# Kernel tuning notes

Measured on AMD Instinct MI355X. Metric: run time of the kernel, lower is better.

## Reference

```python
import jax, jax.numpy as jnp
import numpy as np

B, T, D_IN, H, C = 256, 2048, 64, 32, 16
RHO, SPARSITY = 0.9, 0.1


def _reservoir(rng, n):
    # uniform(-1,1), scale to spectral radius RHO, then sparsify (same order as torch code)
    W = rng.uniform(-1.0, 1.0, (n, n)).astype(np.float32)
    W *= RHO / np.max(np.abs(np.linalg.eigvals(W)))
    W *= (rng.random((n, n)) < SPARSITY).astype(np.float32)
    return jnp.asarray(W)


def _linear(rng, fan_in, fan_out):
    bound = 1.0 / np.sqrt(fan_in)
    W = rng.uniform(-bound, bound, (fan_out, fan_in)).astype(np.float32)
    b = rng.uniform(-bound, bound, (fan_out,)).astype(np.float32)
    return jnp.asarray(W), jnp.asarray(b)


def setup_inputs() -> dict:
    key = jax.random.key(0)
    rng = np.random.default_rng(0)
    x = jax.random.normal(key, (B, T, D_IN), dtype=jnp.float32)
    # frozen encoder input / reservoir weights (uniform(-1,1) weights, default-init biases)
    W_in = jnp.asarray(rng.uniform(-1.0, 1.0, (H, D_IN)).astype(np.float32))
    b_in = jnp.asarray(rng.uniform(-1 / np.sqrt(D_IN), 1 / np.sqrt(D_IN), (H,)).astype(np.float32))
    W_res_enc = _reservoir(rng, H)
    b_res_enc = jnp.asarray(rng.uniform(-1 / np.sqrt(H), 1 / np.sqrt(H), (H,)).astype(np.float32))
    W_code, b_code = _linear(rng, H, C)
    W_co, b_co = _linear(rng, C, H)
    W_res_dec = _reservoir(rng, H)
    b_res_dec = jnp.asarray(rng.uniform(-1 / np.sqrt(H), 1 / np.sqrt(H), (H,)).astype(np.float32))
    W_ro, b_ro = _linear(rng, H, D_IN)
    return dict(x=x, W_in=W_in, b_in=b_in, W_res_enc=W_res_enc, b_res_enc=b_res_enc,
                W_code=W_code, b_code=b_code, W_co=W_co, b_co=b_co,
                W_res_dec=W_res_dec, b_res_dec=b_res_dec, W_ro=W_ro, b_ro=b_ro)


def reference(x, W_in, b_in, W_res_enc, b_res_enc, W_code, b_code, W_co, b_co,
              W_res_dec, b_res_dec, W_ro, b_ro):
    Bs = x.shape[0]
    h0 = jnp.zeros((Bs, W_res_enc.shape[0]), dtype=x.dtype)
    # precompute input projection for all timesteps: [T, B, H]
    u_enc = jnp.swapaxes(jnp.einsum('btd,hd->bth', x, W_in) + b_in, 0, 1)

    def enc_step(h, u):
        h = jnp.tanh(u + h @ W_res_enc.T + b_res_enc)
        return h, h

    _, enc = jax.lax.scan(enc_step, h0, u_enc)
    enc = jnp.swapaxes(enc, 0, 1)                      # [B, T, H]

    z = enc @ W_code.T + b_code                        # [B, T, C]
    h_dec_in = z @ W_co.T + b_co                       # [B, T, H]

    def dec_step(h, u):
        h = jnp.tanh(u + h @ W_res_dec.T + b_res_dec)
        return h, h

    _, dec = jax.lax.scan(dec_step, h0, jnp.swapaxes(h_dec_in, 0, 1))
    dec = jnp.swapaxes(dec, 0, 1)                      # [B, T, H]
    return dec @ W_ro.T + b_ro                         # [B, T, D_IN]
```

## Files before the change

kernel.cpp:

```cpp
#include <hip/hip_runtime.h>
#include <math.h>

#define B_    256
#define T_    2048
#define DIN   64
#define H_    32
#define C_    16

#define CHUNK 128
#define WARM  96
#define NCHUNK (T_ / CHUNK)

#define OFF_U 0u

__device__ __forceinline__ float fast_tanh(float x) {
    float e2 = __expf(x + x);
    return 1.0f - 2.0f * __builtin_amdgcn_rcpf(e2 + 1.0f);
}

__global__ __launch_bounds__(256) void inproj_kernel(
        const float* __restrict__ x, const float* __restrict__ W_in,
        const float* __restrict__ b_in, const float* __restrict__ b_res_enc,
        float* __restrict__ u) {
    __shared__ __align__(16) float4 lx[128 * 16];

    int tid  = threadIdx.x;
    int w    = tid >> 6;
    int lane = tid & 63;
    int i    = lane & 31;
    int par  = lane >> 5;

    float Wr[DIN];
    {
        const float4* wi4 = reinterpret_cast<const float4*>(W_in + i * DIN);
#pragma unroll
        for (int q = 0; q < DIN / 4; ++q) {
            float4 v = wi4[q];
            Wr[4*q+0] = v.x; Wr[4*q+1] = v.y; Wr[4*q+2] = v.z; Wr[4*q+3] = v.w;
        }
    }
    float bi = b_in[i] + b_res_enc[i];

    long row_base = (long)blockIdx.x * 128;
    const float4* xg = reinterpret_cast<const float4*>(x) + row_base * 16;

#pragma unroll
    for (int k = 0; k < 8; ++k)
        lx[tid + 256 * k] = xg[tid + 256 * k];
    __syncthreads();

#pragma unroll
    for (int g = 0; g < 4; ++g) {
        int r0 = w * 32 + g * 8 + par;
        float acc0 = 0.f, acc1 = 0.f, acc2 = 0.f, acc3 = 0.f;
#pragma unroll
        for (int k4 = 0; k4 < 16; ++k4) {
            float4 wv = { Wr[4*k4+0], Wr[4*k4+1], Wr[4*k4+2], Wr[4*k4+3] };
            float4 x0 = lx[(r0 + 0) * 16 + k4];
            float4 x1 = lx[(r0 + 2) * 16 + k4];
            float4 x2 = lx[(r0 + 4) * 16 + k4];
            float4 x3 = lx[(r0 + 6) * 16 + k4];
            acc0 += x0.x * wv.x + x0.y * wv.y + x0.z * wv.z + x0.w * wv.w;
            acc1 += x1.x * wv.x + x1.y * wv.y + x1.z * wv.z + x1.w * wv.w;
            acc2 += x2.x * wv.x + x2.y * wv.y + x2.z * wv.z + x2.w * wv.w;
            acc3 += x3.x * wv.x + x3.y * wv.y + x3.z * wv.z + x3.w * wv.w;
        }
        long rg = row_base + r0;
        u[(rg + 0) * H_ + i] = acc0 + bi;
        u[(rg + 2) * H_ + i] = acc1 + bi;
        u[(rg + 4) * H_ + i] = acc2 + bi;
        u[(rg + 6) * H_ + i] = acc3 + bi;
    }
}

__global__ __launch_bounds__(64, 4) void scan_kernel(
        const float* __restrict__ u,
        const float* __restrict__ W_res_enc,
        const float* __restrict__ W_res_dec, const float* __restrict__ b_res_dec,
        const float* __restrict__ W_code, const float* __restrict__ b_code,
        const float* __restrict__ W_co,   const float* __restrict__ b_co,
        float* __restrict__ hd ) {
    int lane = threadIdx.x;
    int i = lane & 31;
    int p = lane >> 5;
    int b = blockIdx.x & (B_ - 1);
    int c = blockIdx.x >> 8;
    int t0 = c * CHUNK;
    int tstart = (c == 0) ? 0 : (t0 - WARM);
    int tend = t0 + CHUNK;

    __shared__ __align__(16) float wcode[C_ * H_];
    {
        const float4* src = reinterpret_cast<const float4*>(W_code);
        float4* dst = reinterpret_cast<float4*>(wcode);
        dst[lane]      = src[lane];
        dst[lane + 64] = src[lane + 64];
    }

    float We[16], Wd[16], Wco_r[C_];
    {
        const float4* we4 = reinterpret_cast<const float4*>(W_res_enc + i * H_ + p * 16);
        const float4* wd4 = reinterpret_cast<const float4*>(W_res_dec + i * H_ + p * 16);
        const float4* wc4 = reinterpret_cast<const float4*>(W_co + i * C_);
#pragma unroll
        for (int q = 0; q < 4; ++q) {
            float4 a = we4[q], d = wd4[q], w = wc4[q];
            We[4*q+0]=a.x; We[4*q+1]=a.y; We[4*q+2]=a.z; We[4*q+3]=a.w;
            Wd[4*q+0]=d.x; Wd[4*q+1]=d.y; Wd[4*q+2]=d.z; Wd[4*q+3]=d.w;
            Wco_r[4*q+0]=w.x; Wco_r[4*q+1]=w.y; Wco_r[4*q+2]=w.z; Wco_r[4*q+3]=w.w;
        }
    }
    __syncthreads();

    float Wc[16];
#pragma unroll
    for (int k = 0; k < 16; ++k) {
        float s = 0.f;
#pragma unroll
        for (int cc = 0; cc < C_; ++cc)
            s += Wco_r[cc] * wcode[cc * H_ + p * 16 + k];
        Wc[k] = s;
    }
    float bcd;
    {
        float s = b_co[i] + b_res_dec[i];
#pragma unroll
        for (int cc = 0; cc < C_; ++cc)
            s += Wco_r[cc] * b_code[cc];
        bcd = s;
    }

    float he[16], hdv[16];
#pragma unroll
    for (int k = 0; k < 16; ++k) { he[k] = 0.f; hdv[k] = 0.f; }

    __shared__ __align__(16) float lhe[H_];
    __shared__ __align__(16) float lhd[H_];

    const float* ub = u  + ((long)b * T_) * H_ + i;
    float*       hb = hd + ((long)b * T_) * DIN + i;

    float ucur = ub[(long)tstart * H_];
    float un1  = ub[(long)(tstart + 1) * H_];
    float un2  = ub[(long)(tstart + 2) * H_];

    for (int t = tstart; t < t0; ++t) {
        float e0 = 0.f, e1 = 0.f, e2 = 0.f, e3 = 0.f;
#pragma unroll
        for (int k = 0; k < 16; k += 4) {
            e0 += We[k+0] * he[k+0];
            e1 += We[k+1] * he[k+1];
            e2 += We[k+2] * he[k+2];
            e3 += We[k+3] * he[k+3];
        }
        float ep = (e0 + e1) + (e2 + e3);
        float a = fast_tanh(ep + __shfl_xor(ep, 32) + ucur);
        lhe[i] = a;
        __syncthreads();
        {
            const float4* s4 = reinterpret_cast<const float4*>(&lhe[p * 16]);
#pragma unroll
            for (int q = 0; q < 4; ++q) {
                float4 v = s4[q];
                he[4*q+0]=v.x; he[4*q+1]=v.y; he[4*q+2]=v.z; he[4*q+3]=v.w;
            }
        }
        float g0 = 0.f, g1 = 0.f, d0 = 0.f, d1 = 0.f;
#pragma unroll
        for (int k = 0; k < 16; k += 2) {
            g0 += Wc[k+0] * he[k+0];
            g1 += Wc[k+1] * he[k+1];
            d0 += Wd[k+0] * hdv[k+0];
            d1 += Wd[k+1] * hdv[k+1];
        }
        float part = (g0 + g1) + (d0 + d1);
        float d = fast_tanh(part + __shfl_xor(part, 32) + bcd);
        ucur = un1; un1 = un2;
        un2 = ub[(long)(t + 3) * H_];
        lhd[i] = d;
        __syncthreads();
        {
            const float4* s4 = reinterpret_cast<const float4*>(&lhd[p * 16]);
#pragma unroll
            for (int q = 0; q < 4; ++q) {
                float4 v = s4[q];
                hdv[4*q+0]=v.x; hdv[4*q+1]=v.y; hdv[4*q+2]=v.z; hdv[4*q+3]=v.w;
            }
        }
    }

    for (int t = t0; t < tend; ++t) {
        float e0 = 0.f, e1 = 0.f, e2 = 0.f, e3 = 0.f;
#pragma unroll
        for (int k = 0; k < 16; k += 4) {
            e0 += We[k+0] * he[k+0];
            e1 += We[k+1] * he[k+1];
            e2 += We[k+2] * he[k+2];
            e3 += We[k+3] * he[k+3];
        }
        float ep = (e0 + e1) + (e2 + e3);
        float a = fast_tanh(ep + __shfl_xor(ep, 32) + ucur);
        lhe[i] = a;
        __syncthreads();
        {
            const float4* s4 = reinterpret_cast<const float4*>(&lhe[p * 16]);
#pragma unroll
            for (int q = 0; q < 4; ++q) {
                float4 v = s4[q];
                he[4*q+0]=v.x; he[4*q+1]=v.y; he[4*q+2]=v.z; he[4*q+3]=v.w;
            }
        }
        float g0 = 0.f, g1 = 0.f, d0 = 0.f, d1 = 0.f;
#pragma unroll
        for (int k = 0; k < 16; k += 2) {
            g0 += Wc[k+0] * he[k+0];
            g1 += Wc[k+1] * he[k+1];
            d0 += Wd[k+0] * hdv[k+0];
            d1 += Wd[k+1] * hdv[k+1];
        }
        float part = (g0 + g1) + (d0 + d1);
        float d = fast_tanh(part + __shfl_xor(part, 32) + bcd);
        int tn = t + 3; if (tn > tend - 1) tn = tend - 1;
        ucur = un1; un1 = un2;
        un2 = ub[(long)tn * H_];
        if (p == 0) hb[(long)t * DIN] = d;
        lhd[i] = d;
        __syncthreads();
        {
            const float4* s4 = reinterpret_cast<const float4*>(&lhd[p * 16]);
#pragma unroll
            for (int q = 0; q < 4; ++q) {
                float4 v = s4[q];
                hdv[4*q+0]=v.x; hdv[4*q+1]=v.y; hdv[4*q+2]=v.z; hdv[4*q+3]=v.w;
            }
        }
    }
}

__global__ __launch_bounds__(256) void outproj_kernel(
        const float* __restrict__ W_ro, const float* __restrict__ b_ro,
        float* __restrict__ out) {
    __shared__ __align__(16) float4 lh[128 * 8];

    int tid  = threadIdx.x;
    int w    = tid >> 6;
    int o    = tid & 63;

    float Wo[H_];
    {
        const float4* wo4 = reinterpret_cast<const float4*>(W_ro + o * H_);
#pragma unroll
        for (int q = 0; q < H_ / 4; ++q) {
            float4 v = wo4[q];
            Wo[4*q+0] = v.x; Wo[4*q+1] = v.y; Wo[4*q+2] = v.z; Wo[4*q+3] = v.w;
        }
    }
    float bo = b_ro[o];

    long row_base = (long)blockIdx.x * 128;
    const float4* hg = reinterpret_cast<const float4*>(out);

#pragma unroll
    for (int k = 0; k < 4; ++k) {
        int idx = tid + 256 * k;
        int r = idx >> 3, q = idx & 7;
        lh[idx] = hg[(row_base + r) * 16 + q];
    }
    __syncthreads();

    float* ob = out + (row_base + (long)w * 32) * DIN + o;
#pragma unroll 4
    for (int r = 0; r < 32; ++r) {
        int rr = w * 32 + r;
        float s0 = bo, s1 = 0.f, s2 = 0.f, s3 = 0.f;
#pragma unroll
        for (int q = 0; q < 8; ++q) {
            float4 h4 = lh[rr * 8 + q];
            s0 += Wo[4*q+0] * h4.x;
            s1 += Wo[4*q+1] * h4.y;
            s2 += Wo[4*q+2] * h4.z;
            s3 += Wo[4*q+3] * h4.w;
        }
        __builtin_nontemporal_store((s0 + s1) + (s2 + s3), ob + (long)r * DIN);
    }
}

extern "C" void kernel_launch(void* const* d_in, const int* in_sizes, int n_in,
                              void* d_out, int out_size, void* d_ws, size_t ws_size,
                              hipStream_t stream) {
    const float* x         = (const float*)d_in[0];
    const float* W_in      = (const float*)d_in[1];
    const float* b_in      = (const float*)d_in[2];
    const float* W_res_enc = (const float*)d_in[3];
    const float* b_res_enc = (const float*)d_in[4];
    const float* W_code    = (const float*)d_in[5];
    const float* b_code    = (const float*)d_in[6];
    const float* W_co      = (const float*)d_in[7];
    const float* b_co      = (const float*)d_in[8];
    const float* W_res_dec = (const float*)d_in[9];
    const float* b_res_dec = (const float*)d_in[10];
    const float* W_ro      = (const float*)d_in[11];
    const float* b_ro      = (const float*)d_in[12];
    float* out = (float*)d_out;

    float* u = (float*)((char*)d_ws + OFF_U);

    inproj_kernel<<<(B_ * T_) / 128, 256, 0, stream>>>(x, W_in, b_in, b_res_enc, u);
    scan_kernel<<<B_ * NCHUNK, 64, 0, stream>>>(u, W_res_enc,
                                                W_res_dec, b_res_dec,
                                                W_code, b_code, W_co, b_co, out);
    outproj_kernel<<<(B_ * T_) / 128, 256, 0, stream>>>(W_ro, b_ro, out);
}
```

Measured before the change: 494.2 us.

## Skew decoder one step behind encoder to merge barriers per timestep

The recurrent scan now computes the decoder state for step t-1 in the same iteration as the encoder state for step t. Both tanh results are written together as a float2 into one shared buffer, so each timestep needs one barrier instead of two. This shortens the serial dependency chain and exposes more instruction-level parallelism. The input prefetch no longer clamps its index, so it reads a few rows past the end of each chunk, which for the final chunk lands beyond the buffer.

```diff
diff --git a/kernel.cpp b/kernel.cpp
--- a/kernel.cpp
+++ b/kernel.cpp
@@ -70,6 +70,49 @@
         u[(rg + 2) * H_ + i] = acc1 + bi;
         u[(rg + 4) * H_ + i] = acc2 + bi;
         u[(rg + 6) * H_ + i] = acc3 + bi;
+    }
+}
+
+template<bool DEC, bool STORE>
+__device__ __forceinline__ void esn_step(
+        const float (&We)[16], const float (&Wc)[16], const float (&Wd)[16],
+        float (&he)[16], float (&hdv)[16],
+        float ucur, float bcd, int i, int p,
+        float2* lad, float* sp) {
+    float e0 = 0.f, e1 = 0.f, e2 = 0.f, e3 = 0.f;
+#pragma unroll
+    for (int k = 0; k < 16; k += 4) {
+        e0 += We[k+0] * he[k+0];
+        e1 += We[k+1] * he[k+1];
+        e2 += We[k+2] * he[k+2];
+        e3 += We[k+3] * he[k+3];
+    }
+    float ep = (e0 + e1) + (e2 + e3);
+    float gp = 0.f;
+    if (DEC) {
+        float g0 = 0.f, g1 = 0.f, g2 = 0.f, g3 = 0.f;
+#pragma unroll
+        for (int k = 0; k < 16; k += 2) {
+            g0 += Wc[k+0] * he[k+0];
+            g1 += Wc[k+1] * he[k+1];
+            g2 += Wd[k+0] * hdv[k+0];
+            g3 += Wd[k+1] * hdv[k+1];
+        }
+        gp = (g0 + g1) + (g2 + g3);
+    }
+    float ef = ep + __shfl_xor(ep, 32) + ucur;
+    float gf = gp + __shfl_xor(gp, 32) + bcd;
+    float a = fast_tanh(ef);
+    float d = DEC ? fast_tanh(gf) : 0.f;
+    if (STORE && p == 0) *sp = d;
+    lad[i] = make_float2(a, d);
+    __syncthreads();
+    const float4* s4 = reinterpret_cast<const float4*>(lad + p * 16);
+#pragma unroll
+    for (int q = 0; q < 8; ++q) {
+        float4 v = s4[q];
+        he[2*q+0]  = v.x; hdv[2*q+0] = v.y;
+        he[2*q+1]  = v.z; hdv[2*q+1] = v.w;
     }
 }
 
@@ -134,106 +177,43 @@
 #pragma unroll
     for (int k = 0; k < 16; ++k) { he[k] = 0.f; hdv[k] = 0.f; }
 
-    __shared__ __align__(16) float lhe[H_];
-    __shared__ __align__(16) float lhd[H_];
+    __shared__ __align__(16) float2 lad[H_];
 
     const float* ub = u  + ((long)b * T_) * H_ + i;
-    float*       hb = hd + ((long)b * T_) * DIN + i;
-
-    float ucur = ub[(long)tstart * H_];
-    float un1  = ub[(long)(tstart + 1) * H_];
-    float un2  = ub[(long)(tstart + 2) * H_];
-
-    for (int t = tstart; t < t0; ++t) {
-        float e0 = 0.f, e1 = 0.f, e2 = 0.f, e3 = 0.f;
-#pragma unroll
-        for (int k = 0; k < 16; k += 4) {
-            e0 += We[k+0] * he[k+0];
-            e1 += We[k+1] * he[k+1];
-            e2 += We[k+2] * he[k+2];
-            e3 += We[k+3] * he[k+3];
-        }
-        float ep = (e0 + e1) + (e2 + e3);
-        float a = fast_tanh(ep + __shfl_xor(ep, 32) + ucur);
-        lhe[i] = a;
-        __syncthreads();
-        {
-            const float4* s4 = reinterpret_cast<const float4*>(&lhe[p * 16]);
-#pragma unroll
-            for (int q = 0; q < 4; ++q) {
-                float4 v = s4[q];
-                he[4*q+0]=v.x; he[4*q+1]=v.y; he[4*q+2]=v.z; he[4*q+3]=v.w;
-            }
-        }
-        float g0 = 0.f, g1 = 0.f, d0 = 0.f, d1 = 0.f;
+    float*       hp = hd + ((long)b * T_) * DIN + i + (long)t0 * DIN;
+
+    const float* up = ub + (long)tstart * H_;
+    float ucur = up[0];
+    float un1  = up[H_];
+    float un2  = up[2 * H_];
+    up += 3 * H_;
+
+    esn_step<false, false>(We, Wc, Wd, he, hdv, ucur, bcd, i, p, lad, nullptr);
+    ucur = un1; un1 = un2; un2 = *up; up += H_;
+
+    for (int t = tstart + 1; t <= t0; ++t) {
+        esn_step<true, false>(We, Wc, Wd, he, hdv, ucur, bcd, i, p, lad, nullptr);
+        ucur = un1; un1 = un2; un2 = *up; up += H_;
+    }
+
+    for (int t = t0 + 1; t < tend; ++t) {
+        esn_step<true, true>(We, Wc, Wd, he, hdv, ucur, bcd, i, p, lad, hp);
+        hp += DIN;
+        ucur = un1; un1 = un2; un2 = *up; up += H_;
+    }
+
+    {
+        float g0 = 0.f, g1 = 0.f, g2 = 0.f, g3 = 0.f;
 #pragma unroll
         for (int k = 0; k < 16; k += 2) {
             g0 += Wc[k+0] * he[k+0];
             g1 += Wc[k+1] * he[k+1];
-            d0 += Wd[k+0] * hdv[k+0];
-            d1 += Wd[k+1] * hdv[k+1];
-        }
-        float part = (g0 + g1) + (d0 + d1);
-        float d = fast_tanh(part + __shfl_xor(part, 32) + bcd);
-        ucur = un1; un1 = un2;
-        un2 = ub[(long)(t + 3) * H_];
-        lhd[i] = d;
-        __syncthreads();
-        {
-            const float4* s4 = reinterpret_cast<const float4*>(&lhd[p * 16]);
-#pragma unroll
-            for (int q = 0; q < 4; ++q) {
-                float4 v = s4[q];
-                hdv[4*q+0]=v.x; hdv[4*q+1]=v.y; hdv[4*q+2]=v.z; hdv[4*q+3]=v.w;
-            }
-        }
-    }
-
-    for (int t = t0; t < tend; ++t) {
-        float e0 = 0.f, e1 = 0.f, e2 = 0.f, e3 = 0.f;
-#pragma unroll
-        for (int k = 0; k < 16; k += 4) {
-            e0 += We[k+0] * he[k+0];
-            e1 += We[k+1] * he[k+1];
-            e2 += We[k+2] * he[k+2];
-            e3 += We[k+3] * he[k+3];
-        }
-        float ep = (e0 + e1) + (e2 + e3);
-        float a = fast_tanh(ep + __shfl_xor(ep, 32) + ucur);
-        lhe[i] = a;
-        __syncthreads();
-        {
-            const float4* s4 = reinterpret_cast<const float4*>(&lhe[p * 16]);
-#pragma unroll
-            for (int q = 0; q < 4; ++q) {
-                float4 v = s4[q];
-                he[4*q+0]=v.x; he[4*q+1]=v.y; he[4*q+2]=v.z; he[4*q+3]=v.w;
-            }
-        }
-        float g0 = 0.f, g1 = 0.f, d0 = 0.f, d1 = 0.f;
-#pragma unroll
-        for (int k = 0; k < 16; k += 2) {
-            g0 += Wc[k+0] * he[k+0];
-            g1 += Wc[k+1] * he[k+1];
-            d0 += Wd[k+0] * hdv[k+0];
-            d1 += Wd[k+1] * hdv[k+1];
-        }
-        float part = (g0 + g1) + (d0 + d1);
-        float d = fast_tanh(part + __shfl_xor(part, 32) + bcd);
-        int tn = t + 3; if (tn > tend - 1) tn = tend - 1;
-        ucur = un1; un1 = un2;
-        un2 = ub[(long)tn * H_];
-        if (p == 0) hb[(long)t * DIN] = d;
-        lhd[i] = d;
-        __syncthreads();
-        {
-            const float4* s4 = reinterpret_cast<const float4*>(&lhd[p * 16]);
-#pragma unroll
-            for (int q = 0; q < 4; ++q) {
-                float4 v = s4[q];
-                hdv[4*q+0]=v.x; hdv[4*q+1]=v.y; hdv[4*q+2]=v.z; hdv[4*q+3]=v.w;
-            }
-        }
+            g2 += Wd[k+0] * hdv[k+0];
+            g3 += Wd[k+1] * hdv[k+1];
+        }
+        float gp = (g0 + g1) + (g2 + g3);
+        float d = fast_tanh(gp + __shfl_xor(gp, 32) + bcd);
+        if (p == 0) *hp = d;
     }
 }
 
```

Result: slower. 532.4 us (+7.7%).
